# Performance work log

Measured on AMD Instinct MI355X. Metric: run time of the kernel, lower is better.

## Reference

```python
import jax, jax.numpy as jnp
import numpy as np

N_NODES = 50000
N_EDGES = 800000
IN_F = 64
OUT_F = 64


def setup_inputs() -> dict:
    key = jax.random.key(0)
    k_x, k_r, k_c, k_v, k_w, k_b = jax.random.split(key, 6)
    x = jax.random.normal(k_x, (N_NODES, IN_F), dtype=jnp.float32)
    edge_row = jax.random.randint(k_r, (N_EDGES,), 0, N_NODES, dtype=jnp.int32)
    edge_col = jax.random.randint(k_c, (N_EDGES,), 0, N_NODES, dtype=jnp.int32)
    edge_val = jax.random.uniform(k_v, (N_EDGES,), dtype=jnp.float32)
    weight = jax.random.normal(k_w, (IN_F, OUT_F), dtype=jnp.float32) * (2.0 / (IN_F + OUT_F)) ** 0.5
    bias = jax.random.normal(k_b, (OUT_F,), dtype=jnp.float32) * 0.1
    return {"x": x, "edge_row": edge_row, "edge_col": edge_col,
            "edge_val": edge_val, "weight": weight, "bias": bias}


def reference(x, edge_row, edge_col, edge_val, weight, bias):
    # support = x @ W  : dense GEMM  [N, out]
    support = jnp.matmul(x, weight)
    # output = spmm(adj, support): for each edge (r, c, v): out[r] += v * support[c]
    gathered = support[edge_col] * edge_val[:, None]  # [E, out]
    output = jax.ops.segment_sum(gathered, edge_row, num_segments=N_NODES)
    return output + bias
```

## Files before the change

### kernel.cpp

```cpp
#include <hip/hip_runtime.h>
#include <hip/hip_bf16.h>

#define N_NODES 50000
#define N_EDGES 800000
#define NF 64
#define BUCK_SHIFT 5
#define BUCK_SIZE 32
#define NBUK ((N_NODES + BUCK_SIZE - 1) / BUCK_SIZE)
#define CAP 768
#define CHUNK 4096
#define BIN_BLOCKS ((N_EDGES + CHUNK - 1) / CHUNK)
#define GEMM_BLOCKS 828
#define CSTRIDE 16

__global__ __launch_bounds__(256) void produce(
    const float* __restrict__ x, const int* __restrict__ erow,
    const int* __restrict__ ecol, const float* __restrict__ eval,
    const float* __restrict__ w, int* __restrict__ cursor,
    int2* __restrict__ stage1, __hip_bfloat16* __restrict__ support) {
  __shared__ int hist[NBUK];
  __shared__ int base[NBUK];
  __shared__ int lcur[NBUK];
  const int tid = threadIdx.x;
  const int lane = tid & 63;
  const int wave = tid >> 6;

  if (blockIdx.x < BIN_BLOCKS) {
    for (int t = tid; t < NBUK; t += 256) hist[t] = 0;
    __syncthreads();

    const int e0 = blockIdx.x * CHUNK;
    const int e1 = min(e0 + CHUNK, N_EDGES);
    int r[16], c[16];
    float v[16];
    int n = 0;
    for (int e = e0 + tid; e < e1; e += 256) {
      r[n] = erow[e];
      c[n] = ecol[e];
      v[n] = eval[e];
      atomicAdd(&hist[r[n] >> BUCK_SHIFT], 1);
      ++n;
    }
    __syncthreads();

    for (int t = tid; t < NBUK; t += 256) {
      const int cnt = hist[t];
      base[t] = cnt ? t * CAP + atomicAdd(&cursor[t * CSTRIDE], cnt) : 0;
      lcur[t] = 0;
    }
    __syncthreads();

    for (int j = 0; j < n; ++j) {
      const int b = r[j] >> BUCK_SHIFT;
      const int ofs = atomicAdd(&lcur[b], 1);
      const int pos = base[b] + ofs;
      if (pos < (b + 1) * CAP)
        stage1[pos] = make_int2(((r[j] & (BUCK_SIZE - 1)) << 16) | c[j],
                                __float_as_int(v[j]));
    }
  } else {
    float wcol[NF];
#pragma unroll
    for (int k = 0; k < NF; ++k) wcol[k] = w[k * NF + lane];

    const int wid = (blockIdx.x - BIN_BLOCKS) * 4 + wave;
    const int nw = GEMM_BLOCKS * 4;
    for (int row = wid; row < N_NODES; row += nw) {
      const int row_u = __builtin_amdgcn_readfirstlane(row);
      const float* xr = x + (size_t)row_u * NF;
      float a0 = 0.f, a1 = 0.f, a2 = 0.f, a3 = 0.f;
#pragma unroll
      for (int k = 0; k < NF; k += 4) {
        a0 = fmaf(xr[k + 0], wcol[k + 0], a0);
        a1 = fmaf(xr[k + 1], wcol[k + 1], a1);
        a2 = fmaf(xr[k + 2], wcol[k + 2], a2);
        a3 = fmaf(xr[k + 3], wcol[k + 3], a3);
      }
      support[(size_t)row_u * NF + lane] =
          __float2bfloat16((a0 + a1) + (a2 + a3));
    }
  }
}

__global__ __launch_bounds__(256) void spmm_sorted(
    const __hip_bfloat16* __restrict__ support, const int* __restrict__ cursor,
    const int2* __restrict__ stage1, const float* __restrict__ bias,
    float* __restrict__ out) {
  __shared__ int2 raw[CAP];
  __shared__ int2 srt[CAP];
  __shared__ int rcnt[BUCK_SIZE];
  __shared__ int rofs[BUCK_SIZE];
  __shared__ int rcur[BUCK_SIZE];
  const int b = blockIdx.x;
  const int tid = threadIdx.x;
  const int lane = tid & 63;
  const int wave = tid >> 6;

  if (tid < BUCK_SIZE) rcnt[tid] = 0;
  __syncthreads();

  int cnt = cursor[b * CSTRIDE];
  cnt = cnt > CAP ? CAP : cnt;
  const int2* eb = stage1 + (size_t)b * CAP;

  for (int i = tid; i < cnt; i += 256) {
    const int2 m = eb[i];
    raw[i] = m;
    atomicAdd(&rcnt[m.x >> 16], 1);
  }
  __syncthreads();

  if (tid < 64) {
    const int v = (lane < BUCK_SIZE) ? rcnt[lane] : 0;
    int sc = v;
#pragma unroll
    for (int off = 1; off < 32; off <<= 1) {
      const int up = __shfl_up(sc, off, 64);
      if (lane >= off) sc += up;
    }
    if (lane < BUCK_SIZE) {
      rofs[lane] = sc - v;
      rcur[lane] = sc - v;
    }
  }
  __syncthreads();

  for (int i = tid; i < cnt; i += 256) {
    const int2 m = raw[i];
    const int p = atomicAdd(&rcur[m.x >> 16], 1);
    srt[p] = m;
  }
  __syncthreads();

  const int row0 = b << BUCK_SHIFT;
  const float bv = bias[lane];
#pragma unroll
  for (int rr = 0; rr < 8; ++rr) {
    const int rl = wave * 8 + rr;
    const int row = row0 + rl;
    if (row >= N_NODES) break;
    const int s = __builtin_amdgcn_readfirstlane(rofs[rl]);
    const int e = __builtin_amdgcn_readfirstlane(rofs[rl] + rcnt[rl]);
    float a0 = 0.f, a1 = 0.f, a2 = 0.f, a3 = 0.f;
    int i = s;
    for (; i + 4 <= e; i += 4) {
      const int2 m0 = srt[i + 0];
      const int2 m1 = srt[i + 1];
      const int2 m2 = srt[i + 2];
      const int2 m3 = srt[i + 3];
      const float s0 = __bfloat162float(support[(size_t)(m0.x & 0xFFFF) * NF + lane]);
      const float s1 = __bfloat162float(support[(size_t)(m1.x & 0xFFFF) * NF + lane]);
      const float s2 = __bfloat162float(support[(size_t)(m2.x & 0xFFFF) * NF + lane]);
      const float s3 = __bfloat162float(support[(size_t)(m3.x & 0xFFFF) * NF + lane]);
      a0 = fmaf(__int_as_float(m0.y), s0, a0);
      a1 = fmaf(__int_as_float(m1.y), s1, a1);
      a2 = fmaf(__int_as_float(m2.y), s2, a2);
      a3 = fmaf(__int_as_float(m3.y), s3, a3);
    }
    for (; i < e; ++i) {
      const int2 m0 = srt[i];
      a0 = fmaf(__int_as_float(m0.y),
                __bfloat162float(support[(size_t)(m0.x & 0xFFFF) * NF + lane]),
                a0);
    }
    out[(size_t)row * NF + lane] = ((a0 + a1) + (a2 + a3)) + bv;
  }
}

extern "C" void kernel_launch(void* const* d_in, const int* in_sizes, int n_in,
                              void* d_out, int out_size, void* d_ws,
                              size_t ws_size, hipStream_t stream) {
  const float* x = (const float*)d_in[0];
  const int* erow = (const int*)d_in[1];
  const int* ecol = (const int*)d_in[2];
  const float* eval = (const float*)d_in[3];
  const float* w = (const float*)d_in[4];
  const float* bias = (const float*)d_in[5];
  float* out = (float*)d_out;

  char* ws = (char*)d_ws;
  __hip_bfloat16* support = (__hip_bfloat16*)(ws);
  int2* stage1 = (int2*)(ws + 6400000);
  int* cursor = (int*)(ws + 16003072);

  hipMemsetAsync(cursor, 0, NBUK * CSTRIDE * sizeof(int), stream);

  produce<<<BIN_BLOCKS + GEMM_BLOCKS, 256, 0, stream>>>(
      x, erow, ecol, eval, w, cursor, stage1, support);
  spmm_sorted<<<NBUK, 256, 0, stream>>>(support, cursor, stage1, bias, out);
}
```

Measured before the change: 129.7 us.

## Replace global bucket atomics with per-chunk local sort and offset table

Each binning block now counting-sorts its edge chunk in shared memory and writes it contiguously, along with a per-block bucket offset table. This removes the global atomic cursors and the memset. The spmm kernel gathers its bucket's segments from all chunks, using a prefix scan over the table. This trades scattered global writes and atomics for coalesced writes, at the cost of many small strided segment reads per bucket in the consumer and a large shared-memory footprint in produce that lowers occupancy.

```diff
diff --git a/kernel.cpp b/kernel.cpp
--- a/kernel.cpp
+++ b/kernel.cpp
@@ -11,53 +11,83 @@
 #define CHUNK 4096
 #define BIN_BLOCKS ((N_EDGES + CHUNK - 1) / CHUNK)
 #define GEMM_BLOCKS 828
-#define CSTRIDE 16
+#define TABW (NBUK + 1)
+#define PER ((NBUK + 255) / 256)
 
 __global__ __launch_bounds__(256) void produce(
     const float* __restrict__ x, const int* __restrict__ erow,
     const int* __restrict__ ecol, const float* __restrict__ eval,
-    const float* __restrict__ w, int* __restrict__ cursor,
-    int2* __restrict__ stage1, __hip_bfloat16* __restrict__ support) {
-  __shared__ int hist[NBUK];
-  __shared__ int base[NBUK];
-  __shared__ int lcur[NBUK];
+    const float* __restrict__ w, int2* __restrict__ stage1,
+    int* __restrict__ tab, __hip_bfloat16* __restrict__ support) {
+  __shared__ __align__(16) char smem[CHUNK * 8 + NBUK * 4 * 2 + 16];
   const int tid = threadIdx.x;
   const int lane = tid & 63;
   const int wave = tid >> 6;
 
   if (blockIdx.x < BIN_BLOCKS) {
+    int2* sorted = (int2*)smem;
+    int* hist = (int*)(smem + CHUNK * 8);
+    int* lcur = hist + NBUK;
+    int* wsum = lcur + NBUK;
+
     for (int t = tid; t < NBUK; t += 256) hist[t] = 0;
     __syncthreads();
 
     const int e0 = blockIdx.x * CHUNK;
     const int e1 = min(e0 + CHUNK, N_EDGES);
-    int r[16], c[16];
-    float v[16];
-    int n = 0;
+    const int n = e1 - e0;
+    for (int e = e0 + tid; e < e1; e += 256)
+      atomicAdd(&hist[erow[e] >> BUCK_SHIFT], 1);
+    __syncthreads();
+
+    int loc[PER];
+    int tsum = 0;
+    const int i0 = tid * PER;
+#pragma unroll
+    for (int j = 0; j < PER; ++j) {
+      const int idx = i0 + j;
+      const int v = (idx < NBUK) ? hist[idx] : 0;
+      loc[j] = tsum;
+      tsum += v;
+    }
+    int sc = tsum;
+#pragma unroll
+    for (int off = 1; off < 64; off <<= 1) {
+      const int up = __shfl_up(sc, off, 64);
+      if (lane >= off) sc += up;
+    }
+    if (lane == 63) wsum[wave] = sc;
+    __syncthreads();
+    int woff = 0;
+#pragma unroll
+    for (int k = 0; k < 4; ++k) woff += (k < wave) ? wsum[k] : 0;
+    const int texcl = woff + sc - tsum;
+    __syncthreads();
+
+    int* gt = tab + (size_t)blockIdx.x * TABW;
+#pragma unroll
+    for (int j = 0; j < PER; ++j) {
+      const int idx = i0 + j;
+      if (idx < NBUK) {
+        const int o = texcl + loc[j];
+        hist[idx] = o;
+        lcur[idx] = o;
+        gt[idx] = o;
+      }
+    }
+    if (tid == 0) gt[NBUK] = n;
+    __syncthreads();
+
     for (int e = e0 + tid; e < e1; e += 256) {
-      r[n] = erow[e];
-      c[n] = ecol[e];
-      v[n] = eval[e];
-      atomicAdd(&hist[r[n] >> BUCK_SHIFT], 1);
-      ++n;
-    }
-    __syncthreads();
-
-    for (int t = tid; t < NBUK; t += 256) {
-      const int cnt = hist[t];
-      base[t] = cnt ? t * CAP + atomicAdd(&cursor[t * CSTRIDE], cnt) : 0;
-      lcur[t] = 0;
-    }
-    __syncthreads();
-
-    for (int j = 0; j < n; ++j) {
-      const int b = r[j] >> BUCK_SHIFT;
-      const int ofs = atomicAdd(&lcur[b], 1);
-      const int pos = base[b] + ofs;
-      if (pos < (b + 1) * CAP)
-        stage1[pos] = make_int2(((r[j] & (BUCK_SIZE - 1)) << 16) | c[j],
-                                __float_as_int(v[j]));
-    }
+      const int r = erow[e];
+      const int p = atomicAdd(&lcur[r >> BUCK_SHIFT], 1);
+      sorted[p] = make_int2(((r & (BUCK_SIZE - 1)) << 16) | ecol[e],
+                            __float_as_int(eval[e]));
+    }
+    __syncthreads();
+
+    int2* gs = stage1 + (size_t)blockIdx.x * CHUNK;
+    for (int i = tid; i < n; i += 256) gs[i] = sorted[i];
   } else {
     float wcol[NF];
 #pragma unroll
@@ -83,7 +113,7 @@
 }
 
 __global__ __launch_bounds__(256) void spmm_sorted(
-    const __hip_bfloat16* __restrict__ support, const int* __restrict__ cursor,
+    const __hip_bfloat16* __restrict__ support, const int* __restrict__ tab,
     const int2* __restrict__ stage1, const float* __restrict__ bias,
     float* __restrict__ out) {
   __shared__ int2 raw[CAP];
@@ -91,36 +121,58 @@
   __shared__ int rcnt[BUCK_SIZE];
   __shared__ int rofs[BUCK_SIZE];
   __shared__ int rcur[BUCK_SIZE];
+  __shared__ int wsum[4];
+  __shared__ int cnt_s;
   const int b = blockIdx.x;
   const int tid = threadIdx.x;
   const int lane = tid & 63;
   const int wave = tid >> 6;
 
   if (tid < BUCK_SIZE) rcnt[tid] = 0;
-  __syncthreads();
-
-  int cnt = cursor[b * CSTRIDE];
+
+  int st = 0, c = 0;
+  if (tid < BIN_BLOCKS) {
+    const int* gt = tab + (size_t)tid * TABW;
+    st = gt[b];
+    c = gt[b + 1] - st;
+  }
+  int sc = c;
+#pragma unroll
+  for (int off = 1; off < 64; off <<= 1) {
+    const int up = __shfl_up(sc, off, 64);
+    if (lane >= off) sc += up;
+  }
+  if (lane == 63) wsum[wave] = sc;
+  __syncthreads();
+  int woff = 0;
+#pragma unroll
+  for (int k = 0; k < 4; ++k) woff += (k < wave) ? wsum[k] : 0;
+  const int pos = woff + sc - c;
+  if (tid == 255) cnt_s = woff + sc;
+  if (pos + c > CAP) c = max(0, CAP - pos);
+
+  const int2* seg = stage1 + (size_t)tid * CHUNK + st;
+  for (int k = 0; k < c; ++k) {
+    const int2 m = seg[k];
+    raw[pos + k] = m;
+    atomicAdd(&rcnt[m.x >> 16], 1);
+  }
+  __syncthreads();
+
+  int cnt = cnt_s;
   cnt = cnt > CAP ? CAP : cnt;
-  const int2* eb = stage1 + (size_t)b * CAP;
-
-  for (int i = tid; i < cnt; i += 256) {
-    const int2 m = eb[i];
-    raw[i] = m;
-    atomicAdd(&rcnt[m.x >> 16], 1);
-  }
-  __syncthreads();
 
   if (tid < 64) {
     const int v = (lane < BUCK_SIZE) ? rcnt[lane] : 0;
-    int sc = v;
+    int s2 = v;
 #pragma unroll
     for (int off = 1; off < 32; off <<= 1) {
-      const int up = __shfl_up(sc, off, 64);
-      if (lane >= off) sc += up;
+      const int up = __shfl_up(s2, off, 64);
+      if (lane >= off) s2 += up;
     }
     if (lane < BUCK_SIZE) {
-      rofs[lane] = sc - v;
-      rcur[lane] = sc - v;
+      rofs[lane] = s2 - v;
+      rcur[lane] = s2 - v;
     }
   }
   __syncthreads();
@@ -181,11 +233,9 @@
   char* ws = (char*)d_ws;
   __hip_bfloat16* support = (__hip_bfloat16*)(ws);
   int2* stage1 = (int2*)(ws + 6400000);
-  int* cursor = (int*)(ws + 16003072);
-
-  hipMemsetAsync(cursor, 0, NBUK * CSTRIDE * sizeof(int), stream);
+  int* tab = (int*)(ws + 12822528);
 
   produce<<<BIN_BLOCKS + GEMM_BLOCKS, 256, 0, stream>>>(
-      x, erow, ecol, eval, w, cursor, stage1, support);
-  spmm_sorted<<<NBUK, 256, 0, stream>>>(support, cursor, stage1, bias, out);
+      x, erow, ecol, eval, w, stage1, tab, support);
+  spmm_sorted<<<NBUK, 256, 0, stream>>>(support, tab, stage1, bias, out);
 }
```

After: 145.0 us. 1.12x slower.
